# Performance work log

Measured on AMD Instinct MI355X. Metric: run time of the kernel, lower is better.

## Reference

```python
import jax, jax.numpy as jnp
import numpy as np

S = 8192; HID = 2048; H = 16; D = 128; BLK = 256; NC = S // BLK
GROUPS = 8; EPS = 1e-5; ROPE_THETA = 600000.0
LAYER_ID = 0; NLAYERS = 20
SCALE = D ** -0.5

def _build_slopes():
    # ALiBi-style slopes (H is a power of 2), scaled by layer decay factor
    start = 2.0 ** (-2.0 ** (-(np.log2(H) - 3.0)))
    slopes = np.array([start * start ** i for i in range(H)], dtype=np.float32)
    return slopes * np.float32(1.0 - LAYER_ID / (NLAYERS - 1) + 1e-5)

SLOPES = jnp.asarray(_build_slopes())  # [H]

def _rmsnorm(x, w, eps=EPS):
    return x * jax.lax.rsqrt(jnp.mean(x * x, axis=-1, keepdims=True) + eps) * w

def _rope(x, positions):
    # neox-style rotary, x: [S, H, D]
    half = D // 2
    inv_freq = 1.0 / (ROPE_THETA ** (jnp.arange(0, D, 2, dtype=jnp.float32) / D))
    freqs = positions.astype(jnp.float32)[:, None] * inv_freq  # [S, half]
    cos = jnp.cos(freqs)[:, None, :]
    sin = jnp.sin(freqs)[:, None, :]
    x1, x2 = x[..., :half], x[..., half:]
    return jnp.concatenate([x1 * cos - x2 * sin, x2 * cos + x1 * sin], axis=-1)

def _lightning_attn(q, k, v):
    # chunked recurrent linear attention with per-head exponential decay
    # q,k,v: [S, H, D] fp32 -> [S, H*D]
    qc = q.reshape(NC, BLK, H, D).transpose(0, 2, 1, 3)  # [NC, H, BLK, D]
    kc = k.reshape(NC, BLK, H, D).transpose(0, 2, 1, 3)
    vc = v.reshape(NC, BLK, H, D).transpose(0, 2, 1, 3)
    idx = jnp.arange(BLK, dtype=jnp.float32)
    q_decay = jnp.exp(-SLOPES[:, None, None] * (idx + 1.0)[None, :, None])       # [H,BLK,1]
    k_decay = jnp.exp(-SLOPES[:, None, None] * (BLK - 1.0 - idx)[None, :, None])  # [H,BLK,1]
    blk_decay = jnp.exp(-SLOPES * BLK)[:, None, None]                             # [H,1,1]
    dif = idx[:, None] - idx[None, :]
    causal = dif >= 0
    diag_decay = jnp.where(causal, jnp.exp(-SLOPES[:, None, None] * jnp.where(causal, dif, 0.0)), 0.0)  # [H,BLK,BLK]

    def step(kv, inp):
        qb, kb, vb = inp  # each [H, BLK, D]
        qk = jnp.einsum('hid,hjd->hij', qb, kb) * diag_decay
        intra = jnp.einsum('hij,hjd->hid', qk, vb)
        inter = jnp.einsum('hid,hde->hie', qb * q_decay, kv)
        kv_new = blk_decay * kv + jnp.einsum('hjd,hje->hde', kb * k_decay, vb)
        return kv_new, intra + inter

    kv0 = jnp.zeros((H, D, D), dtype=jnp.float32)
    _, out = jax.lax.scan(step, kv0, (qc, kc, vc))  # out: [NC, H, BLK, D]
    return out.transpose(0, 2, 1, 3).reshape(S, H * D)

def setup_inputs() -> dict:
    key = jax.random.key(0)
    ks = jax.random.split(key, 6)
    return {
        'hidden_states': jax.random.normal(ks[0], (S, HID), jnp.float32),
        'positions': jnp.arange(S, dtype=jnp.int32),
        'qkv_w': jax.random.normal(ks[1], (3 * H * D, HID), jnp.float32) * 0.02,
        'qkv_b': jax.random.normal(ks[2], (3 * H * D,), jnp.float32) * 0.01,
        'q_norm_w': jnp.ones((D,), jnp.float32),
        'k_norm_w': jnp.ones((D,), jnp.float32),
        'g_w': jax.random.normal(ks[3], (H * D, HID), jnp.float32) * 0.02,
        'g_norm_w': jnp.ones((H * D,), jnp.float32),
        'dense_w': jax.random.normal(ks[4], (HID, H * D), jnp.float32) * 0.02,
    }

def reference(hidden_states, positions, qkv_w, qkv_b, q_norm_w, k_norm_w, g_w, g_norm_w, dense_w):
    hs = hidden_states.astype(jnp.float32)
    qkv = hs @ qkv_w.T + qkv_b                      # [S, 3*H*D], fp32 (linear_silu=False)
    q, k, v = jnp.split(qkv, [H * D, 2 * H * D], axis=-1)
    q = q.reshape(S, H, D); k = k.reshape(S, H, D); v = v.reshape(S, H, D)
    q = _rmsnorm(q, q_norm_w)                       # use_qk_norm per-head RMSNorm
    k = _rmsnorm(k, k_norm_w)
    q = _rope(q, positions)                         # linear_rope=True
    k = _rope(k, positions)
    q = q * SCALE                                   # linear_scale (minimax backend)
    attn = _lightning_attn(q, k, v)                 # [S, H*D]
    g = hs @ g_w.T                                  # output gate
    xg = attn.reshape(S, GROUPS, (H * D) // GROUPS)  # group RMSNorm (norm_before_gate)
    rstd = jax.lax.rsqrt(jnp.mean(xg * xg, axis=-1, keepdims=True) + EPS)
    y = (xg * rstd).reshape(S, H * D) * g_norm_w * jax.nn.sigmoid(g)
    return y @ dense_w.T                            # [S, HID]
```

## Files before the change

### kernel.cpp

```cpp
#include <hip/hip_runtime.h>

#define S_LEN 8192
#define HID   2048
#define NH    16
#define HD    128
#define BLKC  256
#define QKV_STRIDE 6144
#define EPSV  1e-5f
#define SCALEF 0.08838834764831845f

typedef unsigned short u16;
typedef unsigned int   u32;
typedef __attribute__((ext_vector_type(8))) short bf16x8;
typedef __attribute__((ext_vector_type(4))) float f32x4;

__device__ __forceinline__ float b2f(u16 u) {
    unsigned int x = ((unsigned int)u) << 16;
    return __uint_as_float(x);
}
__device__ __forceinline__ u16 f2b(float f) {
    unsigned int u = __float_as_uint(f);
    u += 0x7fff + ((u >> 16) & 1);
    return (u16)(u >> 16);
}
__device__ __forceinline__ u32 pack2(float lo, float hi) {
    return (u32)f2b(lo) | ((u32)f2b(hi) << 16);
}
__device__ __forceinline__ float get_slope(int h) {
    return exp2f(-0.5f * (float)(h + 1)) * 1.00001f;
}

#define GLOAD_LDS16(g, l)                                              \
    __builtin_amdgcn_global_load_lds(                                  \
        (const __attribute__((address_space(1))) void*)(g),            \
        (__attribute__((address_space(3))) void*)(l), 16, 0, 0)

#define BARF() do { asm volatile("" ::: "memory");                     \
                    __builtin_amdgcn_s_barrier();                      \
                    asm volatile("" ::: "memory"); } while (0)
#define VMW(n) asm volatile("s_waitcnt vmcnt(" #n ")" ::: "memory")

__global__ __launch_bounds__(256) void canonize_kernel(const float* __restrict__ src,
                                                       u16* __restrict__ dst, int n) {
    const int i0 = (blockIdx.x * 256 + threadIdx.x) * 4;
    if (i0 >= n) return;
    const float4 f = *(const float4*)(src + i0);
    ushort4 o;
    o.x = f2b(f.x); o.y = f2b(f.y); o.z = f2b(f.z); o.w = f2b(f.w);
    *(ushort4*)(dst + i0) = o;
}

template<int D, int KH, int MH>
__device__ __forceinline__ void rd_a(const u16* lds, int aoff0, bf16x8 af[4]) {
#pragma unroll
    for (int mm = 0; mm < 4; ++mm)
        af[mm] = *(const bf16x8*)&lds[D * 16384 + KH * 8192 + (MH * 4 + mm) * 512 + aoff0];
}
template<int D, int KH>
__device__ __forceinline__ void rd_b(const u16* lds, int boff0, bf16x8 bf[4]) {
#pragma unroll
    for (int nn = 0; nn < 4; ++nn)
        bf[nn] = *(const bf16x8*)&lds[32768 + D * 16384 + KH * 8192 + nn * 512 + boff0];
}
template<int MH>
__device__ __forceinline__ void mf(const bf16x8 af[4], const bf16x8 bf[4],
                                   f32x4 (&acc)[8][4]) {
    __builtin_amdgcn_s_setprio(1);
#pragma unroll
    for (int mm = 0; mm < 4; ++mm)
#pragma unroll
        for (int nn = 0; nn < 4; ++nn)
            acc[MH * 4 + mm][nn] = __builtin_amdgcn_mfma_f32_16x16x32_bf16(
                af[mm], bf[nn], acc[MH * 4 + mm][nn], 0, 0, 0);
    __builtin_amdgcn_s_setprio(0);
}

__global__ __launch_bounds__(512, 2) void gemm256_fused(const u16* __restrict__ A,
                                                        const u16* __restrict__ qkvw,
                                                        const u16* __restrict__ gw,
                                                        const u16* __restrict__ bias,
                                                        u16* __restrict__ Cq,
                                                        u16* __restrict__ Cg) {
    __shared__ u16 lds[65536];
    const int tid = threadIdx.x;
    const int w = tid >> 6, l = tid & 63;
    const int row0 = blockIdx.y << 8;
    const int col0 = blockIdx.x << 8;
    const bool isq = (blockIdx.x < 24);
    const u16* Bsel = isq ? qkvw : gw;
    const int bcol0 = isq ? col0 : (col0 - 6144);

    const int scol = (((tid & 3) ^ ((tid >> 2) & 3)) << 3);
    const u16* aSrc = A    + (size_t)(row0  + (tid >> 2)) * 2048 + scol;
    const u16* bSrc = Bsel + (size_t)(bcol0 + (tid >> 2)) * 2048 + scol;

#define STAGE_A(d, kh, tk) do {                                                        \
    GLOAD_LDS16(aSrc + (size_t)(tk) * 64 + (kh) * 32,                                  \
                lds + (d) * 16384 + (kh) * 8192 + tid * 8);                            \
    GLOAD_LDS16(aSrc + (size_t)128 * 2048 + (size_t)(tk) * 64 + (kh) * 32,             \
                lds + (d) * 16384 + (kh) * 8192 + 4096 + tid * 8); } while (0)
#define STAGE_B(d, kh, tk) do {                                                        \
    GLOAD_LDS16(bSrc + (size_t)(tk) * 64 + (kh) * 32,                                  \
                lds + 32768 + (d) * 16384 + (kh) * 8192 + tid * 8);                    \
    GLOAD_LDS16(bSrc + (size_t)128 * 2048 + (size_t)(tk) * 64 + (kh) * 32,             \
                lds + 32768 + (d) * 16384 + (kh) * 8192 + 4096 + tid * 8); } while (0)

    const int wr = (w >> 2) << 7;
    const int wc = (w & 3) << 6;
    const int fslot = (((l >> 4) ^ (l & 3)) << 3);
    const int aoff0 = (wr + (l & 15)) * 32 + fslot;
    const int boff0 = (wc + (l & 15)) * 32 + fslot;

    f32x4 acc[8][4] = {};
    bf16x8 af[4], bf[4];

    STAGE_A(0, 0, 0); STAGE_B(0, 0, 0);
    STAGE_A(0, 1, 0); STAGE_B(0, 1, 0);
    STAGE_A(1, 0, 1); STAGE_B(1, 0, 1);

    for (int tk = 0; tk < 30; tk += 2) {
        VMW(8); BARF();
        rd_a<0, 0, 0>(lds, aoff0, af); rd_b<0, 0>(lds, boff0, bf);
        STAGE_A(1, 1, tk + 1);
        BARF(); mf<0>(af, bf, acc);
        BARF();
        rd_a<0, 0, 1>(lds, aoff0, af);
        STAGE_B(1, 1, tk + 1);
        BARF(); mf<1>(af, bf, acc);
        VMW(8); BARF();
        rd_a<0, 1, 0>(lds, aoff0, af); rd_b<0, 1>(lds, boff0, bf);
        STAGE_A(0, 0, tk + 2);
        BARF(); mf<0>(af, bf, acc);
        BARF();
        rd_a<0, 1, 1>(lds, aoff0, af);
        STAGE_B(0, 0, tk + 2);
        BARF(); mf<1>(af, bf, acc);
        VMW(8); BARF();
        rd_a<1, 0, 0>(lds, aoff0, af); rd_b<1, 0>(lds, boff0, bf);
        STAGE_A(0, 1, tk + 2);
        BARF(); mf<0>(af, bf, acc);
        BARF();
        rd_a<1, 0, 1>(lds, aoff0, af);
        STAGE_B(0, 1, tk + 2);
        BARF(); mf<1>(af, bf, acc);
        VMW(8); BARF();
        rd_a<1, 1, 0>(lds, aoff0, af); rd_b<1, 1>(lds, boff0, bf);
        STAGE_A(1, 0, tk + 3);
        BARF(); mf<0>(af, bf, acc);
        BARF();
        rd_a<1, 1, 1>(lds, aoff0, af);
        STAGE_B(1, 0, tk + 3);
        BARF(); mf<1>(af, bf, acc);
    }
    VMW(8); BARF();
    rd_a<0, 0, 0>(lds, aoff0, af); rd_b<0, 0>(lds, boff0, bf);
    STAGE_A(1, 1, 31);
    BARF(); mf<0>(af, bf, acc);
    BARF();
    rd_a<0, 0, 1>(lds, aoff0, af);
    STAGE_B(1, 1, 31);
    BARF(); mf<1>(af, bf, acc);
    VMW(8); BARF();
    rd_a<0, 1, 0>(lds, aoff0, af); rd_b<0, 1>(lds, boff0, bf);
    BARF(); mf<0>(af, bf, acc);
    BARF();
    rd_a<0, 1, 1>(lds, aoff0, af);
    BARF(); mf<1>(af, bf, acc);
    VMW(4); BARF();
    rd_a<1, 0, 0>(lds, aoff0, af); rd_b<1, 0>(lds, boff0, bf);
    BARF(); mf<0>(af, bf, acc);
    BARF();
    rd_a<1, 0, 1>(lds, aoff0, af);
    BARF(); mf<1>(af, bf, acc);
    VMW(0); BARF();
    rd_a<1, 1, 0>(lds, aoff0, af); rd_b<1, 1>(lds, boff0, bf);
    BARF(); mf<0>(af, bf, acc);
    BARF();
    rd_a<1, 1, 1>(lds, aoff0, af);
    BARF(); mf<1>(af, bf, acc);
#undef STAGE_A
#undef STAGE_B

    u16* Cout = isq ? Cq : Cg;
    const int ldc = isq ? 6144 : 2048;
    const int ccb = (isq ? col0 : (col0 - 6144)) + wc + (l & 15);
    const int crb = row0 + wr + ((l >> 4) << 2);
#pragma unroll
    for (int nn = 0; nn < 4; ++nn) {
        const float bv = isq ? b2f(bias[col0 + wc + nn * 16 + (l & 15)]) : 0.f;
#pragma unroll
        for (int mm = 0; mm < 8; ++mm) {
#pragma unroll
            for (int r = 0; r < 4; ++r)
                Cout[(size_t)(crb + mm * 16 + r) * ldc + ccb + nn * 16] =
                    f2b(acc[mm][nn][r] + bv);
        }
    }
}

template<int OUT_F32>
__global__ __launch_bounds__(256) void gemm_mfma(const u16* __restrict__ A,
                                                 const u16* __restrict__ B,
                                                 const u16* __restrict__ bias,
                                                 void* __restrict__ Cv,
                                                 int K, int lda, int ldb, int ldc) {
    __shared__ u16 As[128 * 32];
    __shared__ u16 Bs[128 * 32];
    const int t = threadIdx.x;
    const int w = t >> 6;
    const int l = t & 63;
    const int row0 = blockIdx.y << 7, col0 = blockIdx.x << 7;

    const int se   = (w << 9) + (l << 3);
    const int srow = se >> 5;
    const int scol = se & 31;
    const u16* Ap = A + (size_t)(row0 + srow) * lda + scol;
    const u16* Bp = B + (size_t)(col0 + srow) * ldb + scol;
    u16* AsP = As + se;
    u16* BsP = Bs + se;

    const int wr = (w >> 1) << 6;
    const int wc = (w & 1) << 6;
    const int fr = l & 15;
    const int fk = (l >> 4) << 3;

    f32x4 acc[4][4] = {};

    for (int k0 = 0; k0 < K; k0 += 32) {
        __syncthreads();
        GLOAD_LDS16(Ap + k0, AsP);
        GLOAD_LDS16(Ap + k0 + (size_t)64 * lda, AsP + 64 * 32);
        GLOAD_LDS16(Bp + k0, BsP);
        GLOAD_LDS16(Bp + k0 + (size_t)64 * ldb, BsP + 64 * 32);
        __syncthreads();

        bf16x8 a[4], b[4];
#pragma unroll
        for (int m = 0; m < 4; ++m)
            a[m] = *(const bf16x8*)&As[(wr + (m << 4) + fr) * 32 + fk];
#pragma unroll
        for (int n = 0; n < 4; ++n)
            b[n] = *(const bf16x8*)&Bs[(wc + (n << 4) + fr) * 32 + fk];
#pragma unroll
        for (int m = 0; m < 4; ++m)
#pragma unroll
            for (int n = 0; n < 4; ++n)
                acc[m][n] = __builtin_amdgcn_mfma_f32_16x16x32_bf16(
                    a[m], b[n], acc[m][n], 0, 0, 0);
    }

    const int crow = row0 + wr + ((l >> 4) << 2);
    const int ccol = col0 + wc + fr;
#pragma unroll
    for (int n = 0; n < 4; ++n) {
        const float bv = (bias != nullptr) ? b2f(bias[ccol + (n << 4)]) : 0.f;
#pragma unroll
        for (int m = 0; m < 4; ++m) {
#pragma unroll
            for (int r = 0; r < 4; ++r) {
                const float val = acc[m][n][r] + bv;
                const size_t off = (size_t)(crow + (m << 4) + r) * ldc + ccol + (n << 4);
                if (OUT_F32) ((float*)Cv)[off] = val;
                else         ((u16*)Cv)[off]   = f2b(val);
            }
        }
    }
}

__global__ __launch_bounds__(256) void normrope_kernel(u16* __restrict__ qkvb,
                                                       const u16* __restrict__ qw,
                                                       const u16* __restrict__ kw,
                                                       const int* __restrict__ pos,
                                                       int row0) {
    const int wid = (blockIdx.x << 2) + (threadIdx.x >> 6);
    const int s = wid >> 4, h = wid & 15;
    const int l = threadIdx.x & 63;
    u16* qp = qkvb + (size_t)s * QKV_STRIDE + h * HD;
    u16* kp = qp + HID;
    const float q0 = b2f(qp[l]), q1 = b2f(qp[l + 64]);
    const float k0 = b2f(kp[l]), k1 = b2f(kp[l + 64]);
    float sq = q0 * q0 + q1 * q1;
    float sk = k0 * k0 + k1 * k1;
#pragma unroll
    for (int off = 32; off > 0; off >>= 1) {
        sq += __shfl_xor(sq, off);
        sk += __shfl_xor(sk, off);
    }
    const float qr = rsqrtf(sq * (1.f / 128.f) + EPSV);
    const float kr = rsqrtf(sk * (1.f / 128.f) + EPSV);
    const float nq0 = q0 * qr * b2f(qw[l]), nq1 = q1 * qr * b2f(qw[l + 64]);
    const float nk0 = k0 * kr * b2f(kw[l]), nk1 = k1 * kr * b2f(kw[l + 64]);
    const int p = pos[row0 + s];
    const float invf = powf(600000.f, -(float)l * (1.f / 64.f));
    const float fr = (float)p * invf;
    const float cs = cosf(fr), sn = sinf(fr);
    qp[l]      = f2b((nq0 * cs - nq1 * sn) * SCALEF);
    qp[l + 64] = f2b((nq1 * cs + nq0 * sn) * SCALEF);
    kp[l]      = f2b(nk0 * cs - nk1 * sn);
    kp[l + 64] = f2b(nk1 * cs + nk0 * sn);
}

__global__ __launch_bounds__(256) void kv_contrib_kernel(const u16* __restrict__ qkvb,
                                                         float* __restrict__ contrib) {
    const int b = blockIdx.x;
    const int eh = b & 1;
    const int h = (b >> 1) & 15;
    const int c = b >> 5;
    const float slope = get_slope(h);
    const u16* kb = qkvb + (size_t)c * BLKC * QKV_STRIDE + HID + h * HD;
    const u16* vb = kb + HID;
    const int t = threadIdx.x;
    const int tx = t & 15, ty = t >> 4;
    const int jj = t >> 5, dd = (t & 31) << 2;
    float acc[4][8] = {};
    __shared__ float kf[8][128], vf[8][128];
    for (int j0 = 0; j0 < BLKC; j0 += 8) {
        const float kd = expf(-slope * (float)(BLKC - 1 - (j0 + jj)));
        ushort4 k4 = *(const ushort4*)(kb + (size_t)(j0 + jj) * QKV_STRIDE + dd);
        ushort4 v4 = *(const ushort4*)(vb + (size_t)(j0 + jj) * QKV_STRIDE + dd);
        kf[jj][dd + 0] = b2f(k4.x) * kd; kf[jj][dd + 1] = b2f(k4.y) * kd;
        kf[jj][dd + 2] = b2f(k4.z) * kd; kf[jj][dd + 3] = b2f(k4.w) * kd;
        vf[jj][dd + 0] = b2f(v4.x); vf[jj][dd + 1] = b2f(v4.y);
        vf[jj][dd + 2] = b2f(v4.z); vf[jj][dd + 3] = b2f(v4.w);
        __syncthreads();
#pragma unroll
        for (int j = 0; j < 8; ++j) {
            float4 e0 = *(const float4*)&vf[j][(eh << 6) + (ty << 2)];
            float4 d0 = *(const float4*)&kf[j][tx << 3];
            float4 d1 = *(const float4*)&kf[j][(tx << 3) + 4];
            float er[4] = {e0.x, e0.y, e0.z, e0.w};
            float dr[8] = {d0.x, d0.y, d0.z, d0.w, d1.x, d1.y, d1.z, d1.w};
#pragma unroll
            for (int u = 0; u < 4; ++u)
#pragma unroll
                for (int v = 0; v < 8; ++v) acc[u][v] += er[u] * dr[v];
        }
        __syncthreads();
    }
    float* cb = contrib + ((size_t)(c * NH + h) * HD + (eh << 6) + (ty << 2)) * HD + (tx << 3);
#pragma unroll
    for (int u = 0; u < 4; ++u) {
        *(float4*)(cb + (size_t)u * HD)     = make_float4(acc[u][0], acc[u][1], acc[u][2], acc[u][3]);
        *(float4*)(cb + (size_t)u * HD + 4) = make_float4(acc[u][4], acc[u][5], acc[u][6], acc[u][7]);
    }
}

__global__ __launch_bounds__(256) void kv_scan_kernel(const float* __restrict__ buf,
                                                      u16* __restrict__ bufb,
                                                      float* __restrict__ carry,
                                                      int ncs) {
    const int tid = blockIdx.x * 256 + threadIdx.x;
    const int h = tid >> 14;
    const float bd = expf(-get_slope(h) * (float)BLKC);
    float prev = carry[tid];
    for (int c = 0; c < ncs; ++c) {
        const size_t off = (size_t)c * (NH * HD * HD) + tid;
        const float cur = buf[off];
        bufb[off] = f2b(prev);
        prev = bd * prev + cur;
    }
    carry[tid] = prev;
}

__global__ __launch_bounds__(256) void attn_mfma_kernel(u16* __restrict__ qkvb,
                                                        const u16* __restrict__ kvstatesb) {
    const int b  = blockIdx.x;
    const int hb = b & 1;
    const int h  = (b >> 1) & 15;
    const int c  = b >> 5;
    const float slope = get_slope(h);
    const int t  = threadIdx.x;
    const int w  = t >> 6, l = t & 63;
    const int lg = l >> 4, lc = l & 15;
    const int giw = hb * 4 + w;
    const int i0  = giw << 5;

    __shared__ u16 Ks[32 * 128];
    __shared__ u16 Vt[128 * 40];
    __shared__ u16 Sb[4 * 1024];

    const u16* qbase = qkvb + (size_t)(c * BLKC) * QKV_STRIDE + h * HD;
    bf16x8 qa[2][4];
#pragma unroll
    for (int m = 0; m < 2; ++m)
#pragma unroll
        for (int kk = 0; kk < 4; ++kk)
            qa[m][kk] = *(const bf16x8*)(qbase +
                (size_t)(i0 + m * 16 + lc) * QKV_STRIDE + kk * 32 + lg * 8);

    f32x4 acc[2][8] = {};

    const u16* kbase = qkvb + (size_t)(c * BLKC) * QKV_STRIDE + HID + h * HD;
    const u16* vbase = kbase + HID;
    const int jtmax = hb * 4 + 4;
    const int ve  = t & 127;
    const int vph = t >> 7;
    u16* SbW = Sb + (w << 10);

    for (int jt = 0; jt < jtmax; ++jt) {
        __syncthreads();
#pragma unroll
        for (int u = 0; u < 2; ++u) {
            const int idx = t + (u << 8);
            const int j = idx >> 4, s = idx & 15;
            const int sp = s ^ (j & 7);
            GLOAD_LDS16(kbase + (size_t)(jt * 32 + j) * QKV_STRIDE + sp * 8,
                        Ks + idx * 8);
        }
        union { int4 q; u16 e[8]; } vv[2];
#pragma unroll
        for (int u = 0; u < 2; ++u) {
            const int p0 = vph * 8 + u * 16;
#pragma unroll
            for (int x = 0; x < 8; ++x) {
                const int p = p0 + x;
                const int j = ((p & 1) << 4) | (p >> 1);
                vv[u].e[x] = vbase[(size_t)(jt * 32 + j) * QKV_STRIDE + ve];
            }
        }
#pragma unroll
        for (int u = 0; u < 2; ++u) {
            const int p0 = vph * 8 + u * 16;
            *(int4*)&Vt[ve * 40 + p0] = vv[u].q;
        }
        __syncthreads();

        if (jt <= giw) {
            f32x4 sacc[2][2] = {};
#pragma unroll
            for (int kk = 0; kk < 4; ++kk) {
#pragma unroll
                for (int nj = 0; nj < 2; ++nj) {
                    const int j = nj * 16 + lc;
                    const int sp = (kk * 4 + lg) ^ (j & 7);
                    bf16x8 kf = *(const bf16x8*)&Ks[j * 128 + sp * 8];
#pragma unroll
                    for (int m = 0; m < 2; ++m)
                        sacc[m][nj] = __builtin_amdgcn_mfma_f32_16x16x32_bf16(
                            qa[m][kk], kf, sacc[m][nj], 0, 0, 0);
                }
            }
            const int di0 = i0 - jt * 32;
            const float cj0 = expf(slope * (float)lc);
            const float cj1 = expf(slope * (float)(16 + lc));
            const bool diag = (jt == giw);
#pragma unroll
            for (int m = 0; m < 2; ++m) {
#pragma unroll
                for (int r = 0; r < 4; ++r) {
                    const int irel = m * 16 + lg * 4 + r;
                    const float rex = expf(-slope * (float)(di0 + irel));
                    float v0 = sacc[m][0][r] * rex * cj0;
                    float v1 = sacc[m][1][r] * rex * cj1;
                    if (diag) {
                        if (irel < lc)      v0 = 0.f;
                        if (irel < 16 + lc) v1 = 0.f;
                    }
                    const u32 pk = pack2(v0, v1);
                    const int iL = irel;
                    const int rp = iL ^ ((iL >> 2) & 1);
                    *(u32*)&SbW[rp * 32 + ((lc << 1) ^ (((iL >> 2) & 3) << 3))] = pk;
                }
            }
            bf16x8 sA[2];
#pragma unroll
            for (int m = 0; m < 2; ++m) {
                const int iL = m * 16 + lc;
                const int rp = iL ^ ((iL >> 2) & 1);
                sA[m] = *(const bf16x8*)&SbW[rp * 32 + ((lg << 3) ^ (((iL >> 2) & 3) << 3))];
            }
#pragma unroll
            for (int ne = 0; ne < 8; ++ne) {
                bf16x8 vf = *(const bf16x8*)&Vt[(ne * 16 + lc) * 40 + lg * 8];
#pragma unroll
                for (int m = 0; m < 2; ++m)
                    acc[m][ne] = __builtin_amdgcn_mfma_f32_16x16x32_bf16(
                        sA[m], vf, acc[m][ne], 0, 0, 0);
            }
        }
    }

    const u16* kvpb = kvstatesb + (size_t)(c * NH + h) * (HD * HD);
    const float dR0 = expf(-slope * (float)(i0 + lc + 1));
    const float dR1 = expf(-slope * (float)(i0 + 16 + lc + 1));
#pragma unroll
    for (int kk = 0; kk < 4; ++kk) {
        bf16x8 qd[2];
#pragma unroll
        for (int m = 0; m < 2; ++m) {
            const float dR = m ? dR1 : dR0;
            union { bf16x8 v; u32 u[4]; } qq;
            const u16* qe = (const u16*)&qa[m][kk];
#pragma unroll
            for (int x = 0; x < 4; ++x)
                qq.u[x] = pack2(b2f(qe[2 * x]) * dR, b2f(qe[2 * x + 1]) * dR);
            qd[m] = qq.v;
        }
#pragma unroll
        for (int ne = 0; ne < 8; ++ne) {
            bf16x8 kv = *(const bf16x8*)(kvpb + (size_t)(ne * 16 + lc) * HD + kk * 32 + lg * 8);
#pragma unroll
            for (int m = 0; m < 2; ++m)
                acc[m][ne] = __builtin_amdgcn_mfma_f32_16x16x32_bf16(
                    qd[m], kv, acc[m][ne], 0, 0, 0);
        }
    }

    u16* ob = qkvb + (size_t)(c * BLKC) * QKV_STRIDE + h * HD;
#pragma unroll
    for (int m = 0; m < 2; ++m)
#pragma unroll
        for (int ne = 0; ne < 8; ++ne)
#pragma unroll
            for (int r = 0; r < 4; ++r)
                ob[(size_t)(i0 + m * 16 + lg * 4 + r) * QKV_STRIDE + ne * 16 + lc] =
                    f2b(acc[m][ne][r]);
}

__global__ __launch_bounds__(256) void gate_kernel(u16* __restrict__ qkvb,
                                                   const u16* __restrict__ gbuf,
                                                   const u16* __restrict__ gnw) {
    const int s = blockIdx.x;
    const int t = threadIdx.x;
    const int j = t << 3;
    const size_t base = (size_t)s * QKV_STRIDE;
    union { int4 v; u16 e[8]; } xr, gr, wv;
    xr.v = *(const int4*)(qkvb + base + j);
    gr.v = *(const int4*)(gbuf + (size_t)s * 2048 + j);
    wv.v = *(const int4*)(gnw + j);
    float x[8];
    float ss = 0.f;
#pragma unroll
    for (int i = 0; i < 8; ++i) { x[i] = b2f(xr.e[i]); ss += x[i] * x[i]; }
#pragma unroll
    for (int off = 16; off > 0; off >>= 1) ss += __shfl_xor(ss, off, 32);
    const float rstd = rsqrtf(ss * (1.f / 256.f) + EPSV);
    union { int4 v; u16 e[8]; } o;
#pragma unroll
    for (int i = 0; i < 8; ++i) {
        const float yv = x[i] * rstd * b2f(wv.e[i]) *
                         (1.f / (1.f + expf(-b2f(gr.e[i]))));
        o.e[i] = f2b(yv);
    }
    *(int4*)(qkvb + base + 2 * HID + j) = o.v;
}

extern "C" void kernel_launch(void* const* d_in, const int* in_sizes, int n_in,
                              void* d_out, int out_size, void* d_ws, size_t ws_size,
                              hipStream_t stream) {
    const int* pos = (const int*)d_in[1];
    float* out = (float*)d_out;
    char* ws = (char*)d_ws;

    u16*  c_hs    = (u16*)(ws + 256);
    u16*  c_qkvw  = c_hs   + 16777216;
    u16*  c_qkvb  = c_qkvw + 12582912;
    u16*  c_qn    = c_qkvb + 6144;
    u16*  c_kn    = c_qn   + 128;
    u16*  c_gw    = c_kn   + 128;
    u16*  c_gnw   = c_gw   + 4194304;
    u16*  c_dw    = c_gnw  + 2048;
    const size_t canon_end = 256 + (size_t)2 * (16777216 + 12582912 + 6144 + 128 + 128 + 4194304 + 2048 + 4194304);
    const size_t work_off = (canon_end + 255) & ~(size_t)255;

    const size_t MB = 1048576;
    int SCR;
    if      (ws_size >= work_off + 48 * MB) SCR = 2048;
    else if (ws_size >= work_off + 14 * MB) SCR = 512;
    else                                     SCR = 256;
    const int NCS = SCR / BLKC;
    const int NSC = S_LEN / SCR;

    u16*   qkvb    = (u16*)(ws + work_off);
    float* states  = (float*)(ws + work_off + (size_t)SCR * QKV_STRIDE * 2);
    float* carry   = states + (size_t)NCS * NH * HD * HD;
    u16*   statesb = (u16*)(carry + (size_t)NH * HD * HD);
    u16*   gbuf    = statesb + (size_t)NCS * NH * HD * HD;

    const dim3 B256(256);

    canonize_kernel<<<dim3(16777216 / 1024), B256, 0, stream>>>((const float*)d_in[0], c_hs,   16777216);
    canonize_kernel<<<dim3(12582912 / 1024), B256, 0, stream>>>((const float*)d_in[2], c_qkvw, 12582912);
    canonize_kernel<<<dim3(6),               B256, 0, stream>>>((const float*)d_in[3], c_qkvb, 6144);
    canonize_kernel<<<dim3(1),               B256, 0, stream>>>((const float*)d_in[4], c_qn,   128);
    canonize_kernel<<<dim3(1),               B256, 0, stream>>>((const float*)d_in[5], c_kn,   128);
    canonize_kernel<<<dim3(4194304 / 1024),  B256, 0, stream>>>((const float*)d_in[6], c_gw,   4194304);
    canonize_kernel<<<dim3(2),               B256, 0, stream>>>((const float*)d_in[7], c_gnw,  2048);
    canonize_kernel<<<dim3(4194304 / 1024),  B256, 0, stream>>>((const float*)d_in[8], c_dw,   4194304);

    hipMemsetAsync(carry, 0, (size_t)NH * HD * HD * sizeof(float), stream);

    for (int sc = 0; sc < NSC; ++sc) {
        const int row0 = sc * SCR;
        const u16* hsb = c_hs + (size_t)row0 * HID;
        gemm256_fused<<<dim3(32, SCR / 256), dim3(512), 0, stream>>>(
            hsb, c_qkvw, c_gw, c_qkvb, qkvb, gbuf);
        normrope_kernel<<<dim3(SCR * NH / 4), B256, 0, stream>>>(
            qkvb, c_qn, c_kn, pos, row0);
        kv_contrib_kernel<<<dim3(NCS * NH * 2), B256, 0, stream>>>(qkvb, states);
        kv_scan_kernel<<<dim3(NH * HD * HD / 256), B256, 0, stream>>>(states, statesb, carry, NCS);
        attn_mfma_kernel<<<dim3(NCS * NH * 2), B256, 0, stream>>>(qkvb, statesb);
        gate_kernel<<<dim3(SCR), B256, 0, stream>>>(qkvb, gbuf, c_gnw);
        gemm_mfma<1><<<dim3(HID / 128, SCR / 128), B256, 0, stream>>>(
            qkvb + 2 * HID, c_dw, nullptr, out + (size_t)row0 * HID,
            HID, QKV_STRIDE, HID, HID);
    }
}
```

Before: 1.020 ms.

## Swap MFMA operands for row-contiguous vector stores and re-swizzle LDS layout

Both GEMM kernels now pass the MFMA operands in swapped order. This transposes the accumulator fragment so each lane holds four consecutive output columns, and the epilogue can write them as one ushort4/float4 store with a vectorised bias load instead of four strided scalar stores. The LDS XOR swizzle for staging and fragment reads is changed to reduce bank conflicts, and gemm_mfma gains an extra trailing barrier per k-step. Correctness now depends on the new swizzle patterns matching between writers and readers.

```diff
diff --git a/kernel.cpp b/kernel.cpp
--- a/kernel.cpp
+++ b/kernel.cpp
@@ -71,7 +71,7 @@
 #pragma unroll
         for (int nn = 0; nn < 4; ++nn)
             acc[MH * 4 + mm][nn] = __builtin_amdgcn_mfma_f32_16x16x32_bf16(
-                af[mm], bf[nn], acc[MH * 4 + mm][nn], 0, 0, 0);
+                bf[nn], af[mm], acc[MH * 4 + mm][nn], 0, 0, 0);
     __builtin_amdgcn_s_setprio(0);
 }
 
@@ -90,7 +90,7 @@
     const u16* Bsel = isq ? qkvw : gw;
     const int bcol0 = isq ? col0 : (col0 - 6144);
 
-    const int scol = (((tid & 3) ^ ((tid >> 2) & 3)) << 3);
+    const int scol = (((tid & 3) ^ ((tid >> 3) & 3)) << 3);
     const u16* aSrc = A    + (size_t)(row0  + (tid >> 2)) * 2048 + scol;
     const u16* bSrc = Bsel + (size_t)(bcol0 + (tid >> 2)) * 2048 + scol;
 
@@ -107,7 +107,7 @@
 
     const int wr = (w >> 2) << 7;
     const int wc = (w & 3) << 6;
-    const int fslot = (((l >> 4) ^ (l & 3)) << 3);
+    const int fslot = ((((l >> 4) ^ (l >> 1)) & 3) << 3);
     const int aoff0 = (wr + (l & 15)) * 32 + fslot;
     const int boff0 = (wc + (l & 15)) * 32 + fslot;
 
@@ -183,17 +183,23 @@
 
     u16* Cout = isq ? Cq : Cg;
     const int ldc = isq ? 6144 : 2048;
-    const int ccb = (isq ? col0 : (col0 - 6144)) + wc + (l & 15);
-    const int crb = row0 + wr + ((l >> 4) << 2);
+    const int crb = row0 + wr + (l & 15);
+    const int ccb = wc + ((l >> 4) << 2);
 #pragma unroll
     for (int nn = 0; nn < 4; ++nn) {
-        const float bv = isq ? b2f(bias[col0 + wc + nn * 16 + (l & 15)]) : 0.f;
+        float bv[4] = {0.f, 0.f, 0.f, 0.f};
+        if (isq) {
+            ushort4 b4 = *(const ushort4*)(bias + col0 + ccb + nn * 16);
+            bv[0] = b2f(b4.x); bv[1] = b2f(b4.y); bv[2] = b2f(b4.z); bv[3] = b2f(b4.w);
+        }
 #pragma unroll
         for (int mm = 0; mm < 8; ++mm) {
-#pragma unroll
-            for (int r = 0; r < 4; ++r)
-                Cout[(size_t)(crb + mm * 16 + r) * ldc + ccb + nn * 16] =
-                    f2b(acc[mm][nn][r] + bv);
+            ushort4 o;
+            o.x = f2b(acc[mm][nn][0] + bv[0]);
+            o.y = f2b(acc[mm][nn][1] + bv[1]);
+            o.z = f2b(acc[mm][nn][2] + bv[2]);
+            o.w = f2b(acc[mm][nn][3] + bv[3]);
+            *(ushort4*)(Cout + (size_t)(crb + mm * 16) * ldc + bcol0 + ccb + nn * 16) = o;
         }
     }
 }
@@ -211,18 +217,17 @@
     const int l = t & 63;
     const int row0 = blockIdx.y << 7, col0 = blockIdx.x << 7;
 
-    const int se   = (w << 9) + (l << 3);
-    const int srow = se >> 5;
-    const int scol = se & 31;
+    const int srow = t >> 2;
+    const int scol = (((t & 3) ^ ((t >> 3) & 3)) << 3);
     const u16* Ap = A + (size_t)(row0 + srow) * lda + scol;
     const u16* Bp = B + (size_t)(col0 + srow) * ldb + scol;
-    u16* AsP = As + se;
-    u16* BsP = Bs + se;
+    u16* AsP = As + t * 8;
+    u16* BsP = Bs + t * 8;
 
     const int wr = (w >> 1) << 6;
     const int wc = (w & 1) << 6;
     const int fr = l & 15;
-    const int fk = (l >> 4) << 3;
+    const int fk = ((((l >> 4) ^ (l >> 1)) & 3) << 3);
 
     f32x4 acc[4][4] = {};
 
@@ -246,22 +251,30 @@
 #pragma unroll
             for (int n = 0; n < 4; ++n)
                 acc[m][n] = __builtin_amdgcn_mfma_f32_16x16x32_bf16(
-                    a[m], b[n], acc[m][n], 0, 0, 0);
-    }
-
-    const int crow = row0 + wr + ((l >> 4) << 2);
-    const int ccol = col0 + wc + fr;
+                    b[n], a[m], acc[m][n], 0, 0, 0);
+        __syncthreads();
+    }
+
+    const int crb = row0 + wr + (l & 15);
+    const int ccb = col0 + wc + ((l >> 4) << 2);
 #pragma unroll
     for (int n = 0; n < 4; ++n) {
-        const float bv = (bias != nullptr) ? b2f(bias[ccol + (n << 4)]) : 0.f;
+        float bv[4] = {0.f, 0.f, 0.f, 0.f};
+        if (bias != nullptr) {
+            ushort4 b4 = *(const ushort4*)(bias + ccb + n * 16);
+            bv[0] = b2f(b4.x); bv[1] = b2f(b4.y); bv[2] = b2f(b4.z); bv[3] = b2f(b4.w);
+        }
 #pragma unroll
         for (int m = 0; m < 4; ++m) {
-#pragma unroll
-            for (int r = 0; r < 4; ++r) {
-                const float val = acc[m][n][r] + bv;
-                const size_t off = (size_t)(crow + (m << 4) + r) * ldc + ccol + (n << 4);
-                if (OUT_F32) ((float*)Cv)[off] = val;
-                else         ((u16*)Cv)[off]   = f2b(val);
+            if (OUT_F32) {
+                float4 o = make_float4(acc[m][n][0] + bv[0], acc[m][n][1] + bv[1],
+                                       acc[m][n][2] + bv[2], acc[m][n][3] + bv[3]);
+                *(float4*)((float*)Cv + (size_t)(crb + (m << 4)) * ldc + ccb + (n << 4)) = o;
+            } else {
+                ushort4 o;
+                o.x = f2b(acc[m][n][0] + bv[0]); o.y = f2b(acc[m][n][1] + bv[1]);
+                o.z = f2b(acc[m][n][2] + bv[2]); o.w = f2b(acc[m][n][3] + bv[3]);
+                *(ushort4*)((u16*)Cv + (size_t)(crb + (m << 4)) * ldc + ccb + (n << 4)) = o;
             }
         }
     }
```

After: 1.010 ms. No clear change (-1.0%).
